# Kernel tuning notes

Measured on AMD Instinct MI355X. Metric: run time of the kernel, lower is better.

Reference implementation:

```python
import jax, jax.numpy as jnp
import numpy as np

H = 512; W = 512; C = 32; B = 2; N = 120000; HEADS = 2; HD = C // HEADS; S = 9
INDEX_SHIFT = jnp.array([[0,0],[-1,0],[1,0],[0,1],[-1,1],[1,1],[0,-1],[-1,-1],[1,-1]], dtype=jnp.int32)


def setup_inputs() -> dict:
    key = jax.random.key(0)
    ks = jax.random.split(key, 20)
    bev_feats = jax.random.normal(ks[0], (B, N, C), jnp.float32)
    coors = []
    for b in range(B):
        perm = jax.random.permutation(ks[1 + b], H * W)[:N]
        coors.append(jnp.stack([perm // W, perm % W], axis=-1))
    bev_coors = jnp.stack(coors).astype(jnp.int32)
    s = 1.0 / np.sqrt(C)
    u = lambda k, shape, lim: jax.random.uniform(k, shape, jnp.float32, -lim, lim)
    return {
        'bev_feats': bev_feats,
        'bev_coors': bev_coors,
        'ln_w': jnp.ones((C,), jnp.float32),
        'ln_b': jnp.zeros((C,), jnp.float32),
        'wq': u(ks[3], (C, C), s), 'bq': u(ks[4], (C,), s),
        'wk': u(ks[5], (C, C), s), 'bk': u(ks[6], (C,), s),
        'wv': u(ks[7], (C, C), s), 'bv': u(ks[8], (C,), s),
        'pos_w': u(ks[9], (C, 2), 1.0 / np.sqrt(2.0)), 'pos_b': u(ks[10], (C,), 1.0 / np.sqrt(2.0)),
        'in_w': u(ks[11], (3 * C, C), s), 'in_b': jnp.zeros((3 * C,), jnp.float32),
        'out_w': u(ks[12], (C, C), s), 'out_b': jnp.zeros((C,), jnp.float32),
    }


def reference(bev_feats, bev_coors, ln_w, ln_b, wq, bq, wk, bk, wv, bv, pos_w, pos_b, in_w, in_b, out_w, out_b):
    def single(feats, coors):
        # LayerNorm (biased var, eps=1e-5)
        mu = feats.mean(-1, keepdims=True)
        var = feats.var(-1, keepdims=True)
        x = (feats - mu) / jnp.sqrt(var + 1e-5) * ln_w + ln_b
        # qkv 1x1 conv == linear
        q = x @ wq.T + bq
        k = x @ wk.T + bk
        v = x @ wv.T + bv
        # dense grid lookup: coord -> voxel index (-1 if empty)
        flat0 = coors[:, 0] * W + coors[:, 1]
        grid = jnp.full((H * W,), -1, jnp.int32).at[flat0].set(jnp.arange(N, dtype=jnp.int32))
        sc = coors[None] + INDEX_SHIFT[:, None]                      # [9,N,2]
        valid = (sc[..., 0] >= 0) & (sc[..., 0] < H) & (sc[..., 1] >= 0) & (sc[..., 1] < W)
        flat = jnp.clip(sc[..., 0], 0, H - 1) * W + jnp.clip(sc[..., 1], 0, W - 1)
        idx = jnp.where(valid, grid[flat], -1)                       # [9,N]
        pos = INDEX_SHIFT.astype(x.dtype) @ pos_w.T + pos_b          # [9,C]
        m = (idx >= 0)[..., None]
        tv = jnp.where(m, v[idx] + pos[:, None, :], 0.0)             # [9,N,C]
        tk = jnp.where(m, k[idx], 0.0)
        keyt = jnp.swapaxes(tk, 0, 1)                                # [N,9,C]
        valt = jnp.swapaxes(tv, 0, 1)
        # tiny MHA: query len 1, kv len 9, 2 heads (dropout inactive at eval)
        qp = q @ in_w[:C].T + in_b[:C]
        kp = keyt @ in_w[C:2 * C].T + in_b[C:2 * C]
        vp = valt @ in_w[2 * C:].T + in_b[2 * C:]
        qh = qp.reshape(N, HEADS, HD)
        kh = kp.reshape(N, S, HEADS, HD)
        vh = vp.reshape(N, S, HEADS, HD)
        attn = jax.nn.softmax(jnp.einsum('nhd,nshd->nhs', qh, kh) / np.sqrt(HD), axis=-1)
        o = jnp.einsum('nhs,nshd->nhd', attn, vh).reshape(N, C)
        o = o @ out_w.T + out_b
        # scatter to pseudo image [C,H,W]
        canvas = jnp.zeros((C, H * W), o.dtype).at[:, flat0].set(o.T)
        return canvas.reshape(C, H, W)
    return jax.vmap(single)(bev_feats, bev_coors)
```

## Files before the change

kernel.cpp:

```cpp
#include <hip/hip_runtime.h>
#include <hip/hip_fp16.h>
#include <cstdio>
#include <cstdint>

#define HH 512
#define WW 512
#define CC 32
#define BB 2
#define NN 120000
#define HWPIX (HH*WW)
#define NPTS (BB*NN)
#define NPIX (BB*HWPIX)
#define NBLK (NPIX/256)

__device__ __forceinline__ void h8_to_f8(float4 raw, float* o) {
    const __half2* h = (const __half2*)&raw;
    #pragma unroll
    for (int i = 0; i < 4; ++i) {
        float2 f = __half22float2(h[i]);
        o[2 * i] = f.x; o[2 * i + 1] = f.y;
    }
}

__global__ __launch_bounds__(256) void prep(const float* __restrict__ wq, const float* __restrict__ wk,
                          const float* __restrict__ wv, const float* __restrict__ in_w,
                          const float* __restrict__ out_w,
                          const float* __restrict__ bq, const float* __restrict__ bk,
                          const float* __restrict__ bv, const float* __restrict__ in_b,
                          const float* __restrict__ pos_w, const float* __restrict__ pos_b,
                          float* __restrict__ M, float* __restrict__ V, int* __restrict__ fmap_i) {
    int blk = blockIdx.x;
    if (blk < 16) {
        int tid = blk * 256 + threadIdx.x;
        int which = tid >> 10;
        int e = tid & 1023;
        int cp = e & 31;
        int j  = e >> 5;
        if (which < 3) {
            const float* w = (which == 0) ? wq : ((which == 1) ? wk : wv);
            const float* Wrow = in_w + (which * 32 + cp) * 32;
            float acc = 0.f;
            #pragma unroll
            for (int t = 0; t < 32; ++t) acc += Wrow[t] * w[t * 32 + j];
            M[which * 1024 + j * 32 + cp] = acc;
        } else {
            M[3 * 1024 + j * 32 + cp] = out_w[cp * 32 + j];
        }
    } else if (blk == 16) {
        int tid = threadIdx.x;
        if (tid < 32) {
            float a = 0.f, b = 0.f, c = 0.f;
            #pragma unroll
            for (int t = 0; t < 32; ++t) {
                a += in_w[tid * 32 + t] * bq[t];
                b += in_w[(32 + tid) * 32 + t] * bk[t];
                c += in_w[(64 + tid) * 32 + t] * bv[t];
            }
            V[tid]      = a + in_b[tid];
            V[32 + tid] = b;
            V[64 + tid] = c;
        } else if (tid < 128) {
            int grp = (tid - 32) >> 5;
            int cp  = tid & 31;
            float acc = 0.f;
            #pragma unroll
            for (int t = 0; t < 32; ++t) {
                float src = (grp == 0) ? pos_w[t * 2 + 0] : ((grp == 1) ? pos_w[t * 2 + 1] : pos_b[t]);
                acc += in_w[(64 + cp) * 32 + t] * src;
            }
            V[96 + grp * 32 + cp] = acc;
        }
    } else {
        int base = (blk - 17) * 2048 + threadIdx.x * 8;
        int4 z = {0, 0, 0, 0};
        *(int4*)(fmap_i + base)     = z;
        *(int4*)(fmap_i + base + 4) = z;
    }
}

__global__ __launch_bounds__(256) void stage1(const float* __restrict__ feats,
                                              const int* __restrict__ coors,
                                              const float* __restrict__ ln_w,
                                              const float* __restrict__ ln_b,
                                              const float* __restrict__ M,
                                              const float* __restrict__ V,
                                              __half* __restrict__ qh,
                                              __half* __restrict__ kvh,
                                              unsigned char* __restrict__ fmap) {
    int gp = blockIdx.x * 256 + threadIdx.x;
    if (gp >= NPTS) return;
    int b = (gp >= NN) ? 1 : 0;
    int2 yx = ((const int2*)coors)[gp];
    int pix = (b << 18) + (yx.x << 9) + yx.y;

    const float* fr = feats + ((size_t)gp << 5);
    float x[32];
    #pragma unroll
    for (int k = 0; k < 8; ++k) ((float4*)x)[k] = ((const float4*)fr)[k];

    float s1 = 0.f, s2 = 0.f;
    #pragma unroll
    for (int j = 0; j < 32; ++j) { s1 += x[j]; s2 += x[j] * x[j]; }
    float mu   = s1 * (1.f / 32.f);
    float var  = s2 * (1.f / 32.f) - mu * mu;
    float rstd = rsqrtf(var + 1e-5f);
    #pragma unroll
    for (int j = 0; j < 32; ++j) x[j] = (x[j] - mu) * rstd * ln_w[j] + ln_b[j];

    const float4* M4 = (const float4*)M;
    const float4* V4 = (const float4*)V;

    float4 a4[8];
    __half2 hbuf[16];

    #pragma unroll
    for (int c = 0; c < 8; ++c) a4[c] = V4[c];
    #pragma unroll
    for (int j = 0; j < 32; ++j) {
        float xv = x[j];
        #pragma unroll
        for (int c = 0; c < 8; ++c) {
            float4 m = M4[j * 8 + c];
            a4[c].x += xv * m.x; a4[c].y += xv * m.y;
            a4[c].z += xv * m.z; a4[c].w += xv * m.w;
        }
    }
    #pragma unroll
    for (int c = 0; c < 8; ++c) {
        hbuf[2 * c]     = __floats2half2_rn(a4[c].x, a4[c].y);
        hbuf[2 * c + 1] = __floats2half2_rn(a4[c].z, a4[c].w);
    }
    {
        float4* qd = (float4*)(qh + ((size_t)pix << 5));
        #pragma unroll
        for (int k = 0; k < 4; ++k) qd[k] = ((float4*)hbuf)[k];
    }

    __half2 kvbuf[32];

    #pragma unroll
    for (int c = 0; c < 8; ++c) a4[c] = V4[8 + c];
    #pragma unroll
    for (int j = 0; j < 32; ++j) {
        float xv = x[j];
        #pragma unroll
        for (int c = 0; c < 8; ++c) {
            float4 m = M4[256 + j * 8 + c];
            a4[c].x += xv * m.x; a4[c].y += xv * m.y;
            a4[c].z += xv * m.z; a4[c].w += xv * m.w;
        }
    }
    #pragma unroll
    for (int c = 0; c < 8; ++c) {
        kvbuf[2 * c]     = __floats2half2_rn(a4[c].x, a4[c].y);
        kvbuf[2 * c + 1] = __floats2half2_rn(a4[c].z, a4[c].w);
    }

    #pragma unroll
    for (int c = 0; c < 8; ++c) a4[c] = V4[16 + c];
    #pragma unroll
    for (int j = 0; j < 32; ++j) {
        float xv = x[j];
        #pragma unroll
        for (int c = 0; c < 8; ++c) {
            float4 m = M4[512 + j * 8 + c];
            a4[c].x += xv * m.x; a4[c].y += xv * m.y;
            a4[c].z += xv * m.z; a4[c].w += xv * m.w;
        }
    }
    #pragma unroll
    for (int c = 0; c < 8; ++c) {
        kvbuf[16 + 2 * c] = __floats2half2_rn(a4[c].x, a4[c].y);
        kvbuf[17 + 2 * c] = __floats2half2_rn(a4[c].z, a4[c].w);
    }

    float4* kd = (float4*)(kvh + ((size_t)pix << 6));
    #pragma unroll
    for (int k = 0; k < 8; ++k) kd[k] = ((float4*)kvbuf)[k];

    fmap[pix] = 1;
}

__global__ __launch_bounds__(256) void stage23(const unsigned char* __restrict__ fmap,
                                               const __half* __restrict__ qh,
                                               const __half* __restrict__ kvh,
                                               const float* __restrict__ M,
                                               const float* __restrict__ V,
                                               const float* __restrict__ in_b,
                                               const float* __restrict__ out_b,
                                               float* __restrict__ out) {
    __shared__ __half2 lso[256 * 17];
    __shared__ int lsp[256];
    __shared__ int woff[4];

    int w = (blockIdx.x & 7) * 256 + (blockIdx.x >> 3);
    int tid = threadIdx.x;
    int pix = w * 256 + tid;

    bool occ = fmap[pix] != 0;
    unsigned long long mask = __ballot(occ);
    int lane = tid & 63, wvi = tid >> 6;
    if (lane == 0) woff[wvi] = __popcll(mask);
    __syncthreads();
    int pre = 0;
    for (int ww = 0; ww < wvi; ++ww) pre += woff[ww];
    int cnt = woff[0] + woff[1] + woff[2] + woff[3];
    int slot = -1;
    if (occ) {
        slot = pre + __popcll(mask & ((1ull << lane) - 1ull));
        lsp[slot] = tid;
    }
    __syncthreads();

    const int DYC[9] = {0,-1,1,0,-1,1,0,-1,1};
    const int DXC[9] = {0,0,0,1,1,1,-1,-1,-1};

    if (tid < cnt) {
        int pixl = w * 256 + lsp[tid];
        int b = pixl >> 18;
        int p = pixl & (HWPIX - 1);
        int y = p >> 9, x = p & 511;

        float qf[32];
        {
            const float4* q4 = (const float4*)(qh + ((size_t)pixl << 5));
            float4 r0 = q4[0], r1 = q4[1], r2 = q4[2], r3 = q4[3];
            h8_to_f8(r0, qf); h8_to_f8(r1, qf + 8); h8_to_f8(r2, qf + 16); h8_to_f8(r3, qf + 24);
        }

        int np[9];
        bool nv[9];
        #pragma unroll
        for (int s = 0; s < 9; ++s) {
            int sy = y + DYC[s], sx = x + DXC[s];
            bool inb = (sy >= 0) & (sy < HH) & (sx >= 0) & (sx < WW);
            int npx = (b << 18) + (sy << 9) + sx;
            np[s] = npx;
            nv[s] = inb ? (fmap[npx] != 0) : false;
        }

        float eb0 = 0.f, eb1 = 0.f;
        #pragma unroll
        for (int c = 0; c < 16; ++c) {
            eb0 += qf[c]      * in_b[32 + c];
            eb1 += qf[16 + c] * in_b[48 + c];
        }

        float lg0[9], lg1[9];
        #pragma unroll
        for (int s = 0; s < 9; ++s) {
            float d0 = eb0, d1 = eb1;
            if (nv[s]) {
                const float4* kp = (const float4*)(kvh + ((size_t)np[s] << 6));
                float kf[32];
                h8_to_f8(kp[0], kf);      h8_to_f8(kp[1], kf + 8);
                h8_to_f8(kp[2], kf + 16); h8_to_f8(kp[3], kf + 24);
                #pragma unroll
                for (int c = 0; c < 16; ++c) {
                    d0 += qf[c]      * kf[c];
                    d1 += qf[16 + c] * kf[16 + c];
                }
            }
            lg0[s] = d0 * 0.25f;
            lg1[s] = d1 * 0.25f;
        }
        float m0 = lg0[0], m1 = lg1[0];
        #pragma unroll
        for (int s = 1; s < 9; ++s) { m0 = fmaxf(m0, lg0[s]); m1 = fmaxf(m1, lg1[s]); }
        float l0 = 0.f, l1 = 0.f;
        #pragma unroll
        for (int s = 0; s < 9; ++s) {
            lg0[s] = __expf(lg0[s] - m0); l0 += lg0[s];
            lg1[s] = __expf(lg1[s] - m1); l1 += lg1[s];
        }

        float o[32];
        #pragma unroll
        for (int c = 0; c < 32; ++c) o[c] = 0.f;
        float wdy0 = 0.f, wdx0 = 0.f, woc0 = 0.f;
        float wdy1 = 0.f, wdx1 = 0.f, woc1 = 0.f;
        #pragma unroll
        for (int s = 0; s < 9; ++s) {
            if (nv[s]) {
                float w0 = lg0[s], w1 = lg1[s];
                const float4* vp = (const float4*)(kvh + ((size_t)np[s] << 6)) + 4;
                float vf[32];
                h8_to_f8(vp[0], vf);      h8_to_f8(vp[1], vf + 8);
                h8_to_f8(vp[2], vf + 16); h8_to_f8(vp[3], vf + 24);
                #pragma unroll
                for (int c = 0; c < 16; ++c) {
                    o[c]      += w0 * vf[c];
                    o[16 + c] += w1 * vf[16 + c];
                }
                wdy0 += w0 * (float)DYC[s]; wdx0 += w0 * (float)DXC[s]; woc0 += w0;
                wdy1 += w1 * (float)DYC[s]; wdx1 += w1 * (float)DXC[s]; woc1 += w1;
            }
        }
        float rl0 = 1.f / l0, rl1 = 1.f / l1;
        #pragma unroll
        for (int c = 0; c < 16; ++c) {
            o[c]      = (o[c]      + wdy0 * V[96 + c]      + wdx0 * V[128 + c]      + woc0 * V[160 + c])      * rl0 + in_b[64 + c];
            o[16 + c] = (o[16 + c] + wdy1 * V[96 + 16 + c] + wdx1 * V[128 + 16 + c] + woc1 * V[160 + 16 + c]) * rl1 + in_b[80 + c];
        }

        float acc[32];
        #pragma unroll
        for (int c = 0; c < 32; ++c) acc[c] = out_b[c];
        #pragma unroll
        for (int j = 0; j < 32; ++j) {
            float vj = o[j];
            #pragma unroll
            for (int c = 0; c < 32; ++c) acc[c] += vj * M[3072 + j * 32 + c];
        }

        __half2* lrow = lso + tid * 17;
        #pragma unroll
        for (int c = 0; c < 16; ++c) lrow[c] = __floats2half2_rn(acc[2 * c], acc[2 * c + 1]);
    }
    __syncthreads();

    int b = pix >> 18;
    int p = pix & (HWPIX - 1);
    float* outb = out + (size_t)b * CC * HWPIX + p;
    if (occ) {
        const __half2* lrow = lso + slot * 17;
        #pragma unroll
        for (int c2 = 0; c2 < 16; ++c2) {
            float2 f = __half22float2(lrow[c2]);
            outb[(2 * c2) * HWPIX]     = f.x;
            outb[(2 * c2 + 1) * HWPIX] = f.y;
        }
    } else {
        #pragma unroll
        for (int cc = 0; cc < 32; ++cc) outb[cc * HWPIX] = 0.f;
    }
}

extern "C" void kernel_launch(void* const* d_in, const int* in_sizes, int n_in,
                              void* d_out, int out_size, void* d_ws, size_t ws_size,
                              hipStream_t stream) {
    const float* feats = (const float*)d_in[0];
    const int*   coors = (const int*)d_in[1];
    const float* ln_w  = (const float*)d_in[2];
    const float* ln_b  = (const float*)d_in[3];
    const float* wq    = (const float*)d_in[4];
    const float* bq    = (const float*)d_in[5];
    const float* wk    = (const float*)d_in[6];
    const float* bk    = (const float*)d_in[7];
    const float* wv    = (const float*)d_in[8];
    const float* bv    = (const float*)d_in[9];
    const float* pos_w = (const float*)d_in[10];
    const float* pos_b = (const float*)d_in[11];
    const float* in_w  = (const float*)d_in[12];
    const float* in_b  = (const float*)d_in[13];
    const float* out_w = (const float*)d_in[14];
    const float* out_b = (const float*)d_in[15];

    float*  M    = (float*)d_ws;
    float*  V    = M + 4096;
    __half* qh   = (__half*)(V + 192);
    __half* kvh  = qh + (size_t)NPIX * 32;
    unsigned char* fmap = (unsigned char*)(kvh + (size_t)NPIX * 64);
    size_t need = (4096 + 192) * 4 + (size_t)NPIX * 96 * 2 + (size_t)NPIX;
    if (ws_size < need) {
        fprintf(stderr, "kernel_launch: ws too small: %zu < %zu\n", ws_size, need);
        return;
    }

    prep<<<81, 256, 0, stream>>>(wq, wk, wv, in_w, out_w, bq, bk, bv, in_b, pos_w, pos_b,
                                 M, V, (int*)fmap);
    stage1<<<(NPTS + 255) / 256, 256, 0, stream>>>(feats, coors, ln_w, ln_b, M, V, qh, kvh, fmap);
    stage23<<<NBLK, 256, 0, stream>>>(fmap, qh, kvh, M, V, in_b, out_b, (float*)d_out);
}
```

Before: 192.6 us.

## Split fused attention/scatter kernel into compaction, dense attention, and scatter passes

Replaces the per-pixel-block fused kernel with three kernels. One compacts occupied pixels into a global list with an atomic counter, one runs attention on that list with full thread utilisation and writes results in place over q, and one scatters to the output canvas. The goal is to remove the idle threads in blocks where few pixels are occupied and the shared-memory staging. The cost is two extra launches plus extra global writes and reads of the intermediate results, and a list order that depends on the atomic, which hurts locality.

```diff
diff --git a/kernel.cpp b/kernel.cpp
--- a/kernel.cpp
+++ b/kernel.cpp
@@ -28,7 +28,8 @@
                           const float* __restrict__ bq, const float* __restrict__ bk,
                           const float* __restrict__ bv, const float* __restrict__ in_b,
                           const float* __restrict__ pos_w, const float* __restrict__ pos_b,
-                          float* __restrict__ M, float* __restrict__ V, int* __restrict__ fmap_i) {
+                          float* __restrict__ M, float* __restrict__ V, int* __restrict__ fmap_i,
+                          int* __restrict__ pcnt) {
     int blk = blockIdx.x;
     if (blk < 16) {
         int tid = blk * 256 + threadIdx.x;
@@ -69,6 +70,8 @@
                 acc += in_w[(64 + cp) * 32 + t] * src;
             }
             V[96 + grp * 32 + cp] = acc;
+        } else if (tid == 128) {
+            *pcnt = 0;
         }
     } else {
         int base = (blk - 17) * 2048 + threadIdx.x * 8;
@@ -181,158 +184,162 @@
     fmap[pix] = 1;
 }
 
-__global__ __launch_bounds__(256) void stage23(const unsigned char* __restrict__ fmap,
-                                               const __half* __restrict__ qh,
-                                               const __half* __restrict__ kvh,
-                                               const float* __restrict__ M,
-                                               const float* __restrict__ V,
-                                               const float* __restrict__ in_b,
-                                               const float* __restrict__ out_b,
-                                               float* __restrict__ out) {
-    __shared__ __half2 lso[256 * 17];
-    __shared__ int lsp[256];
+__global__ __launch_bounds__(256) void stage1b(const unsigned char* __restrict__ fmap,
+                                               int* __restrict__ plist,
+                                               int* __restrict__ pcnt) {
     __shared__ int woff[4];
-
-    int w = (blockIdx.x & 7) * 256 + (blockIdx.x >> 3);
+    __shared__ int wbase;
     int tid = threadIdx.x;
-    int pix = w * 256 + tid;
-
+    int pix = blockIdx.x * 256 + tid;
     bool occ = fmap[pix] != 0;
     unsigned long long mask = __ballot(occ);
-    int lane = tid & 63, wvi = tid >> 6;
-    if (lane == 0) woff[wvi] = __popcll(mask);
+    int lane = tid & 63, wv = tid >> 6;
+    if (lane == 0) woff[wv] = __popcll(mask);
     __syncthreads();
-    int pre = 0;
-    for (int ww = 0; ww < wvi; ++ww) pre += woff[ww];
-    int cnt = woff[0] + woff[1] + woff[2] + woff[3];
-    int slot = -1;
+    if (tid == 0) wbase = atomicAdd(pcnt, woff[0] + woff[1] + woff[2] + woff[3]);
+    __syncthreads();
     if (occ) {
-        slot = pre + __popcll(mask & ((1ull << lane) - 1ull));
-        lsp[slot] = tid;
-    }
-    __syncthreads();
+        int pre = 0;
+        for (int i = 0; i < wv; ++i) pre += woff[i];
+        plist[wbase + pre + __popcll(mask & ((1ull << lane) - 1ull))] = pix;
+    }
+}
+
+__global__ __launch_bounds__(256) void stage2(const int* __restrict__ plist,
+                                              const unsigned char* __restrict__ fmap,
+                                              __half* __restrict__ qh,
+                                              const __half* __restrict__ kvh,
+                                              const float* __restrict__ M,
+                                              const float* __restrict__ V,
+                                              const float* __restrict__ in_b,
+                                              const float* __restrict__ out_b) {
+    int t = blockIdx.x * 256 + threadIdx.x;
+    if (t >= NPTS) return;
+    int pixl = plist[t];
+    int b = pixl >> 18;
+    int p = pixl & (HWPIX - 1);
+    int y = p >> 9, x = p & 511;
 
     const int DYC[9] = {0,-1,1,0,-1,1,0,-1,1};
     const int DXC[9] = {0,0,0,1,1,1,-1,-1,-1};
 
-    if (tid < cnt) {
-        int pixl = w * 256 + lsp[tid];
-        int b = pixl >> 18;
-        int p = pixl & (HWPIX - 1);
-        int y = p >> 9, x = p & 511;
-
-        float qf[32];
-        {
-            const float4* q4 = (const float4*)(qh + ((size_t)pixl << 5));
-            float4 r0 = q4[0], r1 = q4[1], r2 = q4[2], r3 = q4[3];
-            h8_to_f8(r0, qf); h8_to_f8(r1, qf + 8); h8_to_f8(r2, qf + 16); h8_to_f8(r3, qf + 24);
-        }
-
-        int np[9];
-        bool nv[9];
-        #pragma unroll
-        for (int s = 0; s < 9; ++s) {
-            int sy = y + DYC[s], sx = x + DXC[s];
-            bool inb = (sy >= 0) & (sy < HH) & (sx >= 0) & (sx < WW);
-            int npx = (b << 18) + (sy << 9) + sx;
-            np[s] = npx;
-            nv[s] = inb ? (fmap[npx] != 0) : false;
-        }
-
-        float eb0 = 0.f, eb1 = 0.f;
-        #pragma unroll
-        for (int c = 0; c < 16; ++c) {
-            eb0 += qf[c]      * in_b[32 + c];
-            eb1 += qf[16 + c] * in_b[48 + c];
-        }
-
-        float lg0[9], lg1[9];
-        #pragma unroll
-        for (int s = 0; s < 9; ++s) {
-            float d0 = eb0, d1 = eb1;
-            if (nv[s]) {
-                const float4* kp = (const float4*)(kvh + ((size_t)np[s] << 6));
-                float kf[32];
-                h8_to_f8(kp[0], kf);      h8_to_f8(kp[1], kf + 8);
-                h8_to_f8(kp[2], kf + 16); h8_to_f8(kp[3], kf + 24);
-                #pragma unroll
-                for (int c = 0; c < 16; ++c) {
-                    d0 += qf[c]      * kf[c];
-                    d1 += qf[16 + c] * kf[16 + c];
-                }
+    float qf[32];
+    {
+        const float4* q4 = (const float4*)(qh + ((size_t)pixl << 5));
+        float4 r0 = q4[0], r1 = q4[1], r2 = q4[2], r3 = q4[3];
+        h8_to_f8(r0, qf); h8_to_f8(r1, qf + 8); h8_to_f8(r2, qf + 16); h8_to_f8(r3, qf + 24);
+    }
+
+    int np[9];
+    bool nv[9];
+    #pragma unroll
+    for (int s = 0; s < 9; ++s) {
+        int sy = y + DYC[s], sx = x + DXC[s];
+        bool inb = (sy >= 0) & (sy < HH) & (sx >= 0) & (sx < WW);
+        int npx = (b << 18) + (sy << 9) + sx;
+        np[s] = npx;
+        nv[s] = inb ? (fmap[npx] != 0) : false;
+    }
+
+    float eb0 = 0.f, eb1 = 0.f;
+    #pragma unroll
+    for (int c = 0; c < 16; ++c) {
+        eb0 += qf[c]      * in_b[32 + c];
+        eb1 += qf[16 + c] * in_b[48 + c];
+    }
+
+    float lg0[9], lg1[9];
+    #pragma unroll
+    for (int s = 0; s < 9; ++s) {
+        float d0 = eb0, d1 = eb1;
+        if (nv[s]) {
+            const float4* kp = (const float4*)(kvh + ((size_t)np[s] << 6));
+            float kf[32];
+            h8_to_f8(kp[0], kf);      h8_to_f8(kp[1], kf + 8);
+            h8_to_f8(kp[2], kf + 16); h8_to_f8(kp[3], kf + 24);
+            #pragma unroll
+            for (int c = 0; c < 16; ++c) {
+                d0 += qf[c]      * kf[c];
+                d1 += qf[16 + c] * kf[16 + c];
             }
-            lg0[s] = d0 * 0.25f;
-            lg1[s] = d1 * 0.25f;
-        }
-        float m0 = lg0[0], m1 = lg1[0];
-        #pragma unroll
-        for (int s = 1; s < 9; ++s) { m0 = fmaxf(m0, lg0[s]); m1 = fmaxf(m1, lg1[s]); }
-        float l0 = 0.f, l1 = 0.f;
-        #pragma unroll
-        for (int s = 0; s < 9; ++s) {
-            lg0[s] = __expf(lg0[s] - m0); l0 += lg0[s];
-            lg1[s] = __expf(lg1[s] - m1); l1 += lg1[s];
-        }
-
-        float o[32];
-        #pragma unroll
-        for (int c = 0; c < 32; ++c) o[c] = 0.f;
-        float wdy0 = 0.f, wdx0 = 0.f, woc0 = 0.f;
-        float wdy1 = 0.f, wdx1 = 0.f, woc1 = 0.f;
-        #pragma unroll
-        for (int s = 0; s < 9; ++s) {
-            if (nv[s]) {
-                float w0 = lg0[s], w1 = lg1[s];
-                const float4* vp = (const float4*)(kvh + ((size_t)np[s] << 6)) + 4;
-                float vf[32];
-                h8_to_f8(vp[0], vf);      h8_to_f8(vp[1], vf + 8);
-                h8_to_f8(vp[2], vf + 16); h8_to_f8(vp[3], vf + 24);
-                #pragma unroll
-                for (int c = 0; c < 16; ++c) {
-                    o[c]      += w0 * vf[c];
-                    o[16 + c] += w1 * vf[16 + c];
-                }
-                wdy0 += w0 * (float)DYC[s]; wdx0 += w0 * (float)DXC[s]; woc0 += w0;
-                wdy1 += w1 * (float)DYC[s]; wdx1 += w1 * (float)DXC[s]; woc1 += w1;
+        }
+        lg0[s] = d0 * 0.25f;
+        lg1[s] = d1 * 0.25f;
+    }
+    float m0 = lg0[0], m1 = lg1[0];
+    #pragma unroll
+    for (int s = 1; s < 9; ++s) { m0 = fmaxf(m0, lg0[s]); m1 = fmaxf(m1, lg1[s]); }
+    float l0 = 0.f, l1 = 0.f;
+    #pragma unroll
+    for (int s = 0; s < 9; ++s) {
+        lg0[s] = __expf(lg0[s] - m0); l0 += lg0[s];
+        lg1[s] = __expf(lg1[s] - m1); l1 += lg1[s];
+    }
+
+    float o[32];
+    #pragma unroll
+    for (int c = 0; c < 32; ++c) o[c] = 0.f;
+    float wdy0 = 0.f, wdx0 = 0.f, woc0 = 0.f;
+    float wdy1 = 0.f, wdx1 = 0.f, woc1 = 0.f;
+    #pragma unroll
+    for (int s = 0; s < 9; ++s) {
+        if (nv[s]) {
+            float w0 = lg0[s], w1 = lg1[s];
+            const float4* vp = (const float4*)(kvh + ((size_t)np[s] << 6)) + 4;
+            float vf[32];
+            h8_to_f8(vp[0], vf);      h8_to_f8(vp[1], vf + 8);
+            h8_to_f8(vp[2], vf + 16); h8_to_f8(vp[3], vf + 24);
+            #pragma unroll
+            for (int c = 0; c < 16; ++c) {
+                o[c]      += w0 * vf[c];
+                o[16 + c] += w1 * vf[16 + c];
             }
-        }
-        float rl0 = 1.f / l0, rl1 = 1.f / l1;
-        #pragma unroll
-        for (int c = 0; c < 16; ++c) {
-            o[c]      = (o[c]      + wdy0 * V[96 + c]      + wdx0 * V[128 + c]      + woc0 * V[160 + c])      * rl0 + in_b[64 + c];
-            o[16 + c] = (o[16 + c] + wdy1 * V[96 + 16 + c] + wdx1 * V[128 + 16 + c] + woc1 * V[160 + 16 + c]) * rl1 + in_b[80 + c];
-        }
-
-        float acc[32];
-        #pragma unroll
-        for (int c = 0; c < 32; ++c) acc[c] = out_b[c];
-        #pragma unroll
-        for (int j = 0; j < 32; ++j) {
-            float vj = o[j];
-            #pragma unroll
-            for (int c = 0; c < 32; ++c) acc[c] += vj * M[3072 + j * 32 + c];
-        }
-
-        __half2* lrow = lso + tid * 17;
-        #pragma unroll
-        for (int c = 0; c < 16; ++c) lrow[c] = __floats2half2_rn(acc[2 * c], acc[2 * c + 1]);
-    }
-    __syncthreads();
-
+            wdy0 += w0 * (float)DYC[s]; wdx0 += w0 * (float)DXC[s]; woc0 += w0;
+            wdy1 += w1 * (float)DYC[s]; wdx1 += w1 * (float)DXC[s]; woc1 += w1;
+        }
+    }
+    float rl0 = 1.f / l0, rl1 = 1.f / l1;
+    #pragma unroll
+    for (int c = 0; c < 16; ++c) {
+        o[c]      = (o[c]      + wdy0 * V[96 + c]      + wdx0 * V[128 + c]      + woc0 * V[160 + c])      * rl0 + in_b[64 + c];
+        o[16 + c] = (o[16 + c] + wdy1 * V[96 + 16 + c] + wdx1 * V[128 + 16 + c] + woc1 * V[160 + 16 + c]) * rl1 + in_b[80 + c];
+    }
+
+    float acc[32];
+    #pragma unroll
+    for (int c = 0; c < 32; ++c) acc[c] = out_b[c];
+    #pragma unroll
+    for (int j = 0; j < 32; ++j) {
+        float vj = o[j];
+        #pragma unroll
+        for (int c = 0; c < 32; ++c) acc[c] += vj * M[3072 + j * 32 + c];
+    }
+
+    __half2 hbuf[16];
+    #pragma unroll
+    for (int c = 0; c < 16; ++c) hbuf[c] = __floats2half2_rn(acc[2 * c], acc[2 * c + 1]);
+    float4* od = (float4*)(qh + ((size_t)pixl << 5));
+    #pragma unroll
+    for (int k = 0; k < 4; ++k) od[k] = ((float4*)hbuf)[k];
+}
+
+__global__ __launch_bounds__(256) void stage3(const unsigned char* __restrict__ fmap,
+                                              const __half* __restrict__ qh,
+                                              float* __restrict__ out) {
+    int pix = blockIdx.x * 256 + threadIdx.x;
     int b = pix >> 18;
     int p = pix & (HWPIX - 1);
     float* outb = out + (size_t)b * CC * HWPIX + p;
-    if (occ) {
-        const __half2* lrow = lso + slot * 17;
-        #pragma unroll
-        for (int c2 = 0; c2 < 16; ++c2) {
-            float2 f = __half22float2(lrow[c2]);
-            outb[(2 * c2) * HWPIX]     = f.x;
-            outb[(2 * c2 + 1) * HWPIX] = f.y;
-        }
+    if (fmap[pix] != 0) {
+        const float4* o4 = (const float4*)(qh + ((size_t)pix << 5));
+        float4 r0 = o4[0], r1 = o4[1], r2 = o4[2], r3 = o4[3];
+        float of[32];
+        h8_to_f8(r0, of); h8_to_f8(r1, of + 8); h8_to_f8(r2, of + 16); h8_to_f8(r3, of + 24);
+        #pragma unroll
+        for (int c = 0; c < 32; ++c) outb[c * HWPIX] = of[c];
     } else {
         #pragma unroll
-        for (int cc = 0; cc < 32; ++cc) outb[cc * HWPIX] = 0.f;
+        for (int c = 0; c < 32; ++c) outb[c * HWPIX] = 0.f;
     }
 }
 
@@ -361,14 +368,18 @@
     __half* qh   = (__half*)(V + 192);
     __half* kvh  = qh + (size_t)NPIX * 32;
     unsigned char* fmap = (unsigned char*)(kvh + (size_t)NPIX * 64);
-    size_t need = (4096 + 192) * 4 + (size_t)NPIX * 96 * 2 + (size_t)NPIX;
+    int*    plist = (int*)(fmap + NPIX);
+    int*    pcnt  = plist + NPTS;
+    size_t need = (4096 + 192) * 4 + (size_t)NPIX * 96 * 2 + (size_t)NPIX + (size_t)NPTS * 4 + 4;
     if (ws_size < need) {
         fprintf(stderr, "kernel_launch: ws too small: %zu < %zu\n", ws_size, need);
         return;
     }
 
     prep<<<81, 256, 0, stream>>>(wq, wk, wv, in_w, out_w, bq, bk, bv, in_b, pos_w, pos_b,
-                                 M, V, (int*)fmap);
+                                 M, V, (int*)fmap, pcnt);
     stage1<<<(NPTS + 255) / 256, 256, 0, stream>>>(feats, coors, ln_w, ln_b, M, V, qh, kvh, fmap);
-    stage23<<<NBLK, 256, 0, stream>>>(fmap, qh, kvh, M, V, in_b, out_b, (float*)d_out);
-}
+    stage1b<<<NBLK, 256, 0, stream>>>(fmap, plist, pcnt);
+    stage2<<<(NPTS + 255) / 256, 256, 0, stream>>>(plist, fmap, qh, kvh, M, V, in_b, out_b);
+    stage3<<<NBLK, 256, 0, stream>>>(fmap, qh, (float*)d_out);
+}
```

Result: slower. 232.0 us (+20.5%).

## Store q/kv compactly by point index and use int pixel-to-point map

Applied to the files above, without the earlier changes.

Instead of scattering fp16 q/k/v into dense per-pixel buffers with a byte occupancy map, stage1 writes them contiguously by point index and records the point index in a dense int grid initialised to -1. Stage23 looks up neighbour point indices from that grid and gathers q/kv from the compact arrays. This shrinks the feature buffers and makes stage1's writes coalesced, but the occupancy map grows from one byte to four bytes per pixel and neighbour gathers become indirect.

```diff
diff --git a/kernel.cpp b/kernel.cpp
--- a/kernel.cpp
+++ b/kernel.cpp
@@ -28,7 +28,7 @@
                           const float* __restrict__ bq, const float* __restrict__ bk,
                           const float* __restrict__ bv, const float* __restrict__ in_b,
                           const float* __restrict__ pos_w, const float* __restrict__ pos_b,
-                          float* __restrict__ M, float* __restrict__ V, int* __restrict__ fmap_i) {
+                          float* __restrict__ M, float* __restrict__ V, int* __restrict__ gpmap) {
     int blk = blockIdx.x;
     if (blk < 16) {
         int tid = blk * 256 + threadIdx.x;
@@ -71,10 +71,10 @@
             V[96 + grp * 32 + cp] = acc;
         }
     } else {
-        int base = (blk - 17) * 2048 + threadIdx.x * 8;
-        int4 z = {0, 0, 0, 0};
-        *(int4*)(fmap_i + base)     = z;
-        *(int4*)(fmap_i + base + 4) = z;
+        int base = (blk - 17) * 8192 + threadIdx.x * 32;
+        int4 m1 = {-1, -1, -1, -1};
+        #pragma unroll
+        for (int k = 0; k < 8; ++k) *(int4*)(gpmap + base + 4 * k) = m1;
     }
 }
 
@@ -84,9 +84,9 @@
                                               const float* __restrict__ ln_b,
                                               const float* __restrict__ M,
                                               const float* __restrict__ V,
-                                              __half* __restrict__ qh,
-                                              __half* __restrict__ kvh,
-                                              unsigned char* __restrict__ fmap) {
+                                              __half* __restrict__ qg,
+                                              __half* __restrict__ kvg,
+                                              int* __restrict__ gpmap) {
     int gp = blockIdx.x * 256 + threadIdx.x;
     if (gp >= NPTS) return;
     int b = (gp >= NN) ? 1 : 0;
@@ -131,7 +131,7 @@
         hbuf[2 * c + 1] = __floats2half2_rn(a4[c].z, a4[c].w);
     }
     {
-        float4* qd = (float4*)(qh + ((size_t)pix << 5));
+        float4* qd = (float4*)(qg + ((size_t)gp << 5));
         #pragma unroll
         for (int k = 0; k < 4; ++k) qd[k] = ((float4*)hbuf)[k];
     }
@@ -174,16 +174,16 @@
         kvbuf[17 + 2 * c] = __floats2half2_rn(a4[c].z, a4[c].w);
     }
 
-    float4* kd = (float4*)(kvh + ((size_t)pix << 6));
+    float4* kd = (float4*)(kvg + ((size_t)gp << 6));
     #pragma unroll
     for (int k = 0; k < 8; ++k) kd[k] = ((float4*)kvbuf)[k];
 
-    fmap[pix] = 1;
-}
-
-__global__ __launch_bounds__(256) void stage23(const unsigned char* __restrict__ fmap,
-                                               const __half* __restrict__ qh,
-                                               const __half* __restrict__ kvh,
+    gpmap[pix] = gp;
+}
+
+__global__ __launch_bounds__(256) void stage23(const int* __restrict__ gpmap,
+                                               const __half* __restrict__ qg,
+                                               const __half* __restrict__ kvg,
                                                const float* __restrict__ M,
                                                const float* __restrict__ V,
                                                const float* __restrict__ in_b,
@@ -191,13 +191,15 @@
                                                float* __restrict__ out) {
     __shared__ __half2 lso[256 * 17];
     __shared__ int lsp[256];
+    __shared__ int lsg[256];
     __shared__ int woff[4];
 
     int w = (blockIdx.x & 7) * 256 + (blockIdx.x >> 3);
     int tid = threadIdx.x;
     int pix = w * 256 + tid;
 
-    bool occ = fmap[pix] != 0;
+    int mygp = gpmap[pix];
+    bool occ = mygp >= 0;
     unsigned long long mask = __ballot(occ);
     int lane = tid & 63, wvi = tid >> 6;
     if (lane == 0) woff[wvi] = __popcll(mask);
@@ -209,6 +211,7 @@
     if (occ) {
         slot = pre + __popcll(mask & ((1ull << lane) - 1ull));
         lsp[slot] = tid;
+        lsg[slot] = mygp;
     }
     __syncthreads();
 
@@ -217,26 +220,25 @@
 
     if (tid < cnt) {
         int pixl = w * 256 + lsp[tid];
+        int gpl  = lsg[tid];
         int b = pixl >> 18;
         int p = pixl & (HWPIX - 1);
         int y = p >> 9, x = p & 511;
 
         float qf[32];
         {
-            const float4* q4 = (const float4*)(qh + ((size_t)pixl << 5));
+            const float4* q4 = (const float4*)(qg + ((size_t)gpl << 5));
             float4 r0 = q4[0], r1 = q4[1], r2 = q4[2], r3 = q4[3];
             h8_to_f8(r0, qf); h8_to_f8(r1, qf + 8); h8_to_f8(r2, qf + 16); h8_to_f8(r3, qf + 24);
         }
 
-        int np[9];
-        bool nv[9];
+        int ng[9];
         #pragma unroll
         for (int s = 0; s < 9; ++s) {
             int sy = y + DYC[s], sx = x + DXC[s];
             bool inb = (sy >= 0) & (sy < HH) & (sx >= 0) & (sx < WW);
             int npx = (b << 18) + (sy << 9) + sx;
-            np[s] = npx;
-            nv[s] = inb ? (fmap[npx] != 0) : false;
+            ng[s] = inb ? gpmap[npx] : -1;
         }
 
         float eb0 = 0.f, eb1 = 0.f;
@@ -250,8 +252,8 @@
         #pragma unroll
         for (int s = 0; s < 9; ++s) {
             float d0 = eb0, d1 = eb1;
-            if (nv[s]) {
-                const float4* kp = (const float4*)(kvh + ((size_t)np[s] << 6));
+            if (ng[s] >= 0) {
+                const float4* kp = (const float4*)(kvg + ((size_t)ng[s] << 6));
                 float kf[32];
                 h8_to_f8(kp[0], kf);      h8_to_f8(kp[1], kf + 8);
                 h8_to_f8(kp[2], kf + 16); h8_to_f8(kp[3], kf + 24);
@@ -281,9 +283,9 @@
         float wdy1 = 0.f, wdx1 = 0.f, woc1 = 0.f;
         #pragma unroll
         for (int s = 0; s < 9; ++s) {
-            if (nv[s]) {
+            if (ng[s] >= 0) {
                 float w0 = lg0[s], w1 = lg1[s];
-                const float4* vp = (const float4*)(kvh + ((size_t)np[s] << 6)) + 4;
+                const float4* vp = (const float4*)(kvg + ((size_t)ng[s] << 6)) + 4;
                 float vf[32];
                 h8_to_f8(vp[0], vf);      h8_to_f8(vp[1], vf + 8);
                 h8_to_f8(vp[2], vf + 16); h8_to_f8(vp[3], vf + 24);
@@ -358,17 +360,17 @@
 
     float*  M    = (float*)d_ws;
     float*  V    = M + 4096;
-    __half* qh   = (__half*)(V + 192);
-    __half* kvh  = qh + (size_t)NPIX * 32;
-    unsigned char* fmap = (unsigned char*)(kvh + (size_t)NPIX * 64);
-    size_t need = (4096 + 192) * 4 + (size_t)NPIX * 96 * 2 + (size_t)NPIX;
+    __half* qg   = (__half*)(V + 192);
+    __half* kvg  = qg + (size_t)NPTS * 32;
+    int*   gpmap = (int*)(kvg + (size_t)NPTS * 64);
+    size_t need = (4096 + 192) * 4 + (size_t)NPTS * 96 * 2 + (size_t)NPIX * 4;
     if (ws_size < need) {
         fprintf(stderr, "kernel_launch: ws too small: %zu < %zu\n", ws_size, need);
         return;
     }
 
     prep<<<81, 256, 0, stream>>>(wq, wk, wv, in_w, out_w, bq, bk, bv, in_b, pos_w, pos_b,
-                                 M, V, (int*)fmap);
-    stage1<<<(NPTS + 255) / 256, 256, 0, stream>>>(feats, coors, ln_w, ln_b, M, V, qh, kvh, fmap);
-    stage23<<<NBLK, 256, 0, stream>>>(fmap, qh, kvh, M, V, in_b, out_b, (float*)d_out);
-}
+                                 M, V, gpmap);
+    stage1<<<(NPTS + 255) / 256, 256, 0, stream>>>(feats, coors, ln_w, ln_b, M, V, qg, kvg, gpmap);
+    stage23<<<NBLK, 256, 0, stream>>>(gpmap, qg, kvg, M, V, in_b, out_b, (float*)d_out);
+}
```

Measured after the change: 195.4 us. Within noise of the previous version (+1.5%).
